# Performance work log

Measured on AMD Instinct MI355X. Metric: run time of the kernel, lower is better.

The kernel has to match this reference:

```python
import jax, jax.numpy as jnp
import numpy as np

MIN_BIN_WIDTH = 1e-3
MIN_BIN_HEIGHT = 1e-3
MIN_DERIVATIVE = 1e-3
TAIL_BOUND = 1.0
N_POS = 2097152
N_CHANNELS = 8
N_BINS = 128
DEFAULT_INIT = float(np.log(np.exp(1.0 - MIN_DERIVATIVE) - 1.0))


def setup_inputs() -> dict:
    key = jax.random.key(0)
    k1, k2, k3, k4 = jax.random.split(key, 4)
    # positions rescaled to roughly [-1, 1]; include slight tail overshoot
    x = jax.random.uniform(k1, (N_POS, N_CHANNELS), minval=-1.1, maxval=1.1, dtype=jnp.float32)
    uw = DEFAULT_INIT + 0.1 * jax.random.normal(k2, (N_CHANNELS, N_BINS), dtype=jnp.float32)
    uh = DEFAULT_INIT + 0.1 * jax.random.normal(k3, (N_CHANNELS, N_BINS), dtype=jnp.float32)
    ud = DEFAULT_INIT + 0.1 * jax.random.normal(k4, (N_CHANNELS, N_BINS - 1), dtype=jnp.float32)
    return {"x": x, "unnormalized_widths": uw, "unnormalized_heights": uh,
            "unnormalized_derivatives": ud}


def _bin_edges(unnormalized, min_size, left, right):
    # softmax-normalized sizes with a minimum bin size, cumsum -> knot locations
    n_bins = unnormalized.shape[-1]
    sizes = jax.nn.softmax(unnormalized, axis=-1)
    sizes = min_size + (1.0 - min_size * n_bins) * sizes
    cum = jnp.cumsum(sizes, axis=-1)
    cum = jnp.pad(cum, ((0, 0), (1, 0)))
    cum = (right - left) * cum + left
    cum = cum.at[..., 0].set(left).at[..., -1].set(right)
    sizes = cum[..., 1:] - cum[..., :-1]
    return sizes, cum


def _log_prob(x, uw, uh, ud):
    left, right = -TAIL_BOUND, TAIL_BOUND
    bottom, top = -TAIL_BOUND, TAIL_BOUND
    C = uw.shape[0]

    widths, cumwidths = _bin_edges(uw * 10.0, MIN_BIN_WIDTH, left, right)      # (C,B),(C,B+1)
    heights, cumheights = _bin_edges(uh * 10.0, MIN_BIN_HEIGHT, bottom, top)   # (C,B),(C,B+1)
    ud_pad = jnp.pad(ud, ((0, 0), (1, 1)), constant_values=DEFAULT_INIT)       # linear tails
    derivatives = MIN_DERIVATIVE + jax.nn.softplus(ud_pad)                      # (C,B+1)
    delta = heights / widths                                                    # (C,B)

    inside = (x >= left) & (x <= right)
    xc = jnp.clip(x, bottom, top)  # inverse pass searches over cumheights

    edges = cumheights.at[:, -1].add(1e-6)
    # per-channel bin search, memory-light searchsorted
    idx = jax.vmap(lambda e, v: jnp.searchsorted(e, v, side='right'),
                   in_axes=(0, 1), out_axes=1)(edges, xc) - 1                   # (N,C)
    idx = jnp.clip(idx, 0, widths.shape[-1] - 1)

    ch = jnp.arange(C)[None, :]
    icw = cumwidths[ch, idx]
    ibw = widths[ch, idx]
    ich = cumheights[ch, idx]
    ih = heights[ch, idx]
    idl = delta[ch, idx]
    d0 = derivatives[ch, idx]
    d1 = derivatives[ch, idx + 1]

    # quadratic inverse solve (Durkan et al. rational-quadratic spline)
    dy = xc - ich
    t = d0 + d1 - 2.0 * idl
    a = dy * t + ih * (idl - d0)
    b = ih * d0 - dy * t
    c = -idl * dy
    disc = jnp.maximum(b * b - 4.0 * a * c, 0.0)
    root = (2.0 * c) / (-b - jnp.sqrt(disc))
    theta_1m = root * (1.0 - root)
    denom = idl + t * theta_1m
    der_num = (idl ** 2) * (d1 * root ** 2 + 2.0 * idl * theta_1m + d0 * (1.0 - root) ** 2)
    logabsdet = jnp.log(der_num) - 2.0 * jnp.log(denom)
    logdet = jnp.where(inside, -logabsdet, 0.0)  # identity tails -> logdet 0
    return np.log(0.5).astype(np.float32) + logdet


def reference(x, unnormalized_widths, unnormalized_heights, unnormalized_derivatives):
    return _log_prob(x, unnormalized_widths, unnormalized_heights, unnormalized_derivatives)
```

## Files before the change

kernel.cpp:

```cpp
#include <hip/hip_runtime.h>
#include <math.h>


#define NB 128
#define NCH 8
#define NSLOT 1024
#define EP_F 0
#define P4_F 2064
#define HINT_F 6192
#define TAB_FLOATS 8240

__global__ __launch_bounds__(128) void spline_precompute(
    const float* __restrict__ uw, const float* __restrict__ uh,
    const float* __restrict__ ud, float* __restrict__ ws)
{
    const int c = blockIdx.x;
    const int i = threadIdx.x;
    __shared__ float red[128];
    __shared__ float scan[128];
    __shared__ float cum[129];
    __shared__ float wdt[128];
    __shared__ float sdv[129];
    const float DEFAULT_INIT = logf(expf(1.0f - 1e-3f) - 1.0f);

    float v = uw[c * NB + i] * 10.0f;
    red[i] = v; __syncthreads();
    #pragma unroll
    for (int s = 64; s >= 1; s >>= 1) { if (i < s) red[i] = fmaxf(red[i], red[i + s]); __syncthreads(); }
    float ex = expf(v - red[0]);
    __syncthreads();
    red[i] = ex; __syncthreads();
    #pragma unroll
    for (int s = 64; s >= 1; s >>= 1) { if (i < s) red[i] += red[i + s]; __syncthreads(); }
    float sz = 1e-3f + (1.0f - 1e-3f * NB) * (ex / red[0]);
    __syncthreads();
    scan[i] = sz;
    for (int off = 1; off < NB; off <<= 1) {
        __syncthreads();
        float t = (i >= off) ? scan[i - off] : 0.0f;
        __syncthreads();
        scan[i] += t;
    }
    __syncthreads();
    if (i == 0) cum[0] = -1.0f;
    cum[i + 1] = (i == NB - 1) ? 1.0f : fmaf(2.0f, scan[i], -1.0f);
    __syncthreads();
    wdt[i] = cum[i + 1] - cum[i];
    __syncthreads();

    v = uh[c * NB + i] * 10.0f;
    red[i] = v; __syncthreads();
    #pragma unroll
    for (int s = 64; s >= 1; s >>= 1) { if (i < s) red[i] = fmaxf(red[i], red[i + s]); __syncthreads(); }
    ex = expf(v - red[0]);
    __syncthreads();
    red[i] = ex; __syncthreads();
    #pragma unroll
    for (int s = 64; s >= 1; s >>= 1) { if (i < s) red[i] += red[i + s]; __syncthreads(); }
    sz = 1e-3f + (1.0f - 1e-3f * NB) * (ex / red[0]);
    __syncthreads();
    scan[i] = sz;
    for (int off = 1; off < NB; off <<= 1) {
        __syncthreads();
        float t = (i >= off) ? scan[i - off] : 0.0f;
        __syncthreads();
        scan[i] += t;
    }
    __syncthreads();
    if (i == 0) cum[0] = -1.0f;
    cum[i + 1] = (i == NB - 1) ? 1.0f : fmaf(2.0f, scan[i], -1.0f);

    float u0 = (i == 0) ? DEFAULT_INIT : ud[c * (NB - 1) + i - 1];
    sdv[i] = 1e-3f + log1pf(expf(u0));
    if (i == NB - 1) sdv[NB] = 1e-3f + log1pf(expf(DEFAULT_INIT));
    __syncthreads();

    float hh  = cum[i + 1] - cum[i];
    float idl = hh / wdt[i];
    const int o = c * 129 + i;
    float2* g_ep = reinterpret_cast<float2*>(ws + EP_F);
    float4* g_p4 = reinterpret_cast<float4*>(ws + P4_F);

    float e1 = (i == NB - 1) ? (1.0f + 1e-6f) : cum[i + 1];
    g_ep[o] = make_float2(cum[i], e1);
    g_p4[o] = make_float4(hh, idl, sdv[i], sdv[i + 1]);
    if (i == NB - 1) {
        g_ep[o + 1] = make_float2(1.0f, 1.0f + 1e-6f);
        g_p4[o + 1] = make_float4(1.0f, 1.0f, 1.0f, 1.0f);
    }

    unsigned char* g_hint = reinterpret_cast<unsigned char*>(ws + HINT_F);
    for (int s = i; s < NSLOT; s += NB) {
        float left = (float)s * (2.0f / NSLOT) - 1.0f;
        int k = 0;
        #pragma unroll
        for (int st = 64; st >= 1; st >>= 1) {
            int t = k + st;
            if (cum[t] <= left) k = t;
        }
        g_hint[c * NSLOT + s] = (unsigned char)k;
    }
}

__global__ __launch_bounds__(256) void spline_main(
    const float4* __restrict__ x4, float4* __restrict__ out4,
    const float* __restrict__ ws, int npair)
{
    __shared__ __align__(16) float tab[TAB_FLOATS];
    {
        float4* dst = reinterpret_cast<float4*>(tab);
        const float4* src = reinterpret_cast<const float4*>(ws);
        for (int t = threadIdx.x; t < TAB_FLOATS / 4; t += 256) dst[t] = src[t];
    }
    __syncthreads();
    const float2* ep = reinterpret_cast<const float2*>(tab + EP_F);
    const float4* p4 = reinterpret_cast<const float4*>(tab + P4_F);
    const unsigned char* hint = reinterpret_cast<const unsigned char*>(tab + HINT_F);

    const float LOG_HALF = -0.6931471805599453f;
    const float LN2 = 0.6931471805599453f;
    const int stride = gridDim.x * 256;
    for (int i = blockIdx.x * 256 + threadIdx.x; i < npair; i += stride) {
        float4 xa = x4[2 * i];
        float4 xb = x4[2 * i + 1];
        float xs[8] = {xa.x, xa.y, xa.z, xa.w, xb.x, xb.y, xb.z, xb.w};
        float rs[8];
        #pragma unroll
        for (int j = 0; j < 8; ++j) {
            float v = xs[j];
            float xc = fminf(fmaxf(v, -1.0f), 1.0f);
            float lmul = (__builtin_fabsf(v) <= 1.0f) ? LN2 : 0.0f;

            int s = (int)fmaf(xc, (float)(NSLOT / 2), (float)(NSLOT / 2));
            s = (s > NSLOT - 1) ? NSLOT - 1 : s;
            int k = hint[j * NSLOT + s];

            float2 ee = ep[j * 129 + k];
            bool adv = (ee.y <= xc);
            int k2 = k + (adv ? 1 : 0);
            float ich = adv ? ee.y : ee.x;

            float4 p = p4[j * 129 + k2];
            float h = p.x, dl = p.y, d0 = p.z, d1 = p.w;

            float dy  = xc - ich;
            float T   = fmaf(-2.0f, dl, d0 + d1);
            float dyt = dy * T;
            float B   = h * d0;
            float A   = fmaf(h, dl, -B);
            float aa  = dyt + A;
            float bb  = B - dyt;
            float cc  = -dl * dy;
            float m4  = (aa * cc) * -4.0f;
            float disc = fmaxf(fmaf(bb, bb, m4), 0.0f);
            float sq   = __builtin_amdgcn_sqrtf(disc);
            float nb   = -bb - sq;
            float root = __fdividef(cc + cc, nb);
            float omr  = 1.0f - root;
            float th   = root * omr;
            float den  = fmaf(T, th, dl);
            float sdd  = dl - d0;
            float E    = sdd + sdd;
            float inner = fmaf(fmaf(T, root, E), root, d0);
            float q    = __fdividef(dl, den);
            float val  = inner * (q * q);
            rs[j] = fmaf(-lmul, __log2f(val), LOG_HALF);
        }
        out4[2 * i]     = make_float4(rs[0], rs[1], rs[2], rs[3]);
        out4[2 * i + 1] = make_float4(rs[4], rs[5], rs[6], rs[7]);
    }
}

extern "C" void kernel_launch(void* const* d_in, const int* in_sizes, int n_in,
                              void* d_out, int out_size, void* d_ws, size_t ws_size,
                              hipStream_t stream) {
    const float* x  = (const float*)d_in[0];
    const float* uw = (const float*)d_in[1];
    const float* uh = (const float*)d_in[2];
    const float* ud = (const float*)d_in[3];
    float* ws = (float*)d_ws;

    spline_precompute<<<NCH, NB, 0, stream>>>(uw, uh, ud, ws);

    const int npair = out_size / 8;
    spline_main<<<1024, 256, 0, stream>>>(
        (const float4*)x, (float4*)d_out, ws, npair);
}
```

Measured before the change: 47.29 us.

## Software-prefetch next inputs, batch table lookups, and cut divisions in spline solve

```diff
diff --git a/kernel.cpp b/kernel.cpp
--- a/kernel.cpp
+++ b/kernel.cpp
@@ -102,7 +102,7 @@
     }
 }
 
-__global__ __launch_bounds__(256) void spline_main(
+__global__ __launch_bounds__(256, 4) void spline_main(
     const float4* __restrict__ x4, float4* __restrict__ out4,
     const float* __restrict__ ws, int npair)
 {
@@ -119,31 +119,54 @@
 
     const float LOG_HALF = -0.6931471805599453f;
     const float LN2 = 0.6931471805599453f;
+    const int tid = blockIdx.x * 256 + threadIdx.x;
     const int stride = gridDim.x * 256;
-    for (int i = blockIdx.x * 256 + threadIdx.x; i < npair; i += stride) {
-        float4 xa = x4[2 * i];
-        float4 xb = x4[2 * i + 1];
+
+    float4 pfa = x4[2 * tid];
+    float4 pfb = x4[2 * tid + 1];
+
+    for (int i = tid; i < npair; i += stride) {
+        float4 xa = pfa, xb = pfb;
+        int inx = i + stride;
+        inx = (inx < npair) ? inx : i;
+        pfa = x4[2 * inx];
+        pfb = x4[2 * inx + 1];
+
         float xs[8] = {xa.x, xa.y, xa.z, xa.w, xb.x, xb.y, xb.z, xb.w};
-        float rs[8];
+
+        float xq[8];
+        int kk[8];
         #pragma unroll
         for (int j = 0; j < 8; ++j) {
-            float v = xs[j];
-            float xc = fminf(fmaxf(v, -1.0f), 1.0f);
-            float lmul = (__builtin_fabsf(v) <= 1.0f) ? LN2 : 0.0f;
-
+            float xc = fminf(fmaxf(xs[j], -1.0f), 1.0f);
+            xq[j] = xc;
             int s = (int)fmaf(xc, (float)(NSLOT / 2), (float)(NSLOT / 2));
             s = (s > NSLOT - 1) ? NSLOT - 1 : s;
-            int k = hint[j * NSLOT + s];
-
-            float2 ee = ep[j * 129 + k];
-            bool adv = (ee.y <= xc);
-            int k2 = k + (adv ? 1 : 0);
-            float ich = adv ? ee.y : ee.x;
-
-            float4 p = p4[j * 129 + k2];
-            float h = p.x, dl = p.y, d0 = p.z, d1 = p.w;
-
-            float dy  = xc - ich;
+            kk[j] = hint[j * NSLOT + s];
+        }
+
+        float2 ee[8];
+        #pragma unroll
+        for (int j = 0; j < 8; ++j) ee[j] = ep[j * 129 + kk[j]];
+
+        float4 pk[8];
+        float dyv[8], lm[8];
+        #pragma unroll
+        for (int j = 0; j < 8; ++j) {
+            bool adv = (ee[j].y <= xq[j]);
+            int k2 = kk[j] + (adv ? 1 : 0);
+            float ich = adv ? ee[j].y : ee[j].x;
+            dyv[j] = xq[j] - ich;
+            lm[j] = (xs[j] == xq[j]) ? LN2 : 0.0f;
+            pk[j] = p4[j * 129 + k2];
+        }
+
+        float rs[8];
+        #pragma unroll
+        for (int j = 0; j < 8; ++j) {
+            float h = pk[j].x, dl = pk[j].y, d0 = pk[j].z, d1 = pk[j].w;
+            float dy = dyv[j];
+
             float T   = fmaf(-2.0f, dl, d0 + d1);
             float dyt = dy * T;
             float B   = h * d0;
@@ -151,21 +174,26 @@
             float aa  = dyt + A;
             float bb  = B - dyt;
             float cc  = -dl * dy;
-            float m4  = (aa * cc) * -4.0f;
-            float disc = fmaxf(fmaf(bb, bb, m4), 0.0f);
-            float sq   = __builtin_amdgcn_sqrtf(disc);
-            float nb   = -bb - sq;
-            float root = __fdividef(cc + cc, nb);
-            float omr  = 1.0f - root;
-            float th   = root * omr;
-            float den  = fmaf(T, th, dl);
-            float sdd  = dl - d0;
-            float E    = sdd + sdd;
-            float inner = fmaf(fmaf(T, root, E), root, d0);
-            float q    = __fdividef(dl, den);
-            float val  = inner * (q * q);
-            rs[j] = fmaf(-lmul, __log2f(val), LOG_HALF);
-        }
+            float ac  = aa * cc;
+            float disc = fmaxf(fmaf(-4.0f, ac, bb * bb), 0.0f);
+            float sq  = __builtin_amdgcn_sqrtf(disc);
+            float w   = -bb - sq;
+            float u   = cc + cc;
+            float w2  = w * w;
+            float tu  = T * u;
+            float sdd = dl - d0;
+            float E   = sdd + sdd;
+            float t1  = fmaf(E, w, tu);
+            float num = fmaf(t1, u, d0 * w2);
+            float d2  = dl * dl;
+            float numf = (num * w2) * d2;
+            float wmu = w - u;
+            float denb = fmaf(tu, wmu, dl * w2);
+            float den2 = denb * denb;
+            float val = __fdividef(numf, den2);
+            rs[j] = fmaf(-lm[j], __log2f(val), LOG_HALF);
+        }
+
         out4[2 * i]     = make_float4(rs[0], rs[1], rs[2], rs[3]);
         out4[2 * i + 1] = make_float4(rs[4], rs[5], rs[6], rs[7]);
     }
```

Measured after the change: 44.82 us. -5.2%, faster.
